# Performance work log

Measured on AMD Instinct MI355X. Metric: run time of the kernel, lower is better.

Reference implementation:

```python
import jax, jax.numpy as jnp
import numpy as np

# ---- static config (matches init_kwargs) ----
DIM = 192
HEADS = 6
DEPTH = 2
WS = (2, 7, 7)          # window / group size (Gd, Gh, Gw)
SHIFT = (1, 3, 3)       # cyclic shift for the shifted block (ws // 2)
MLP_RATIO = 4
EPS = 1e-5


def _rel_pos_index(ws):
    # same math as Attention.forward's relative_position_index construction
    coords = np.stack(np.meshgrid(np.arange(ws[0]), np.arange(ws[1]), np.arange(ws[2]), indexing='ij'))
    cf = coords.reshape(3, -1)                       # (3, N)
    rel = cf[:, :, None] - cf[:, None, :]            # (3, N, N)
    rel = rel.transpose(1, 2, 0).copy()              # (N, N, 3)
    rel[:, :, 0] += ws[0] - 1
    rel[:, :, 1] += ws[1] - 1
    rel[:, :, 2] += ws[2] - 1
    rel[:, :, 0] *= (2 * ws[1] - 1) * (2 * ws[2] - 1)
    rel[:, :, 1] *= 2 * ws[2] - 1
    return rel.sum(-1).astype(np.int32)              # (N, N)


def _np_window_partition(x, ws):
    b, d, h, w, c = x.shape
    x = x.reshape(b, d // ws[0], ws[0], h // ws[1], ws[1], w // ws[2], ws[2], c)
    return x.transpose(0, 1, 3, 5, 2, 4, 6, 7).reshape(-1, ws[0] * ws[1] * ws[2], c)


def _compute_mask(dims, ws, ss):
    # faithful to compute_mask in the source (mask value 2.0 on cross-region pairs)
    d, h, w = dims
    img_mask = np.zeros((1, d, h, w, 1), dtype=np.float32)
    cnt = 0
    for ds in (slice(-ws[0]), slice(-ws[0], -ss[0]), slice(-ss[0], None)):
        for hs in (slice(-ws[1]), slice(-ws[1], -ss[1]), slice(-ss[1], None)):
            for wsl in (slice(-ws[2]), slice(-ws[2], -ss[2]), slice(-ss[2], None)):
                img_mask[:, ds, hs, wsl, :] = cnt
                cnt += 1
    mw = _np_window_partition(img_mask, ws).squeeze(-1)   # (nW, N)
    am = mw[:, None, :] - mw[:, :, None]                  # (nW, N, N)
    return np.where(am != 0, np.float32(2.0), np.float32(0.0))


RPI = _rel_pos_index(WS)  # (N, N) int32, constant


def _ln(x, g, b):
    mu = jnp.mean(x, axis=-1, keepdims=True)
    var = jnp.mean(jnp.square(x - mu), axis=-1, keepdims=True)
    return (x - mu) * jax.lax.rsqrt(var + EPS) * g + b


def _win_part(x, ws):
    b, d, h, w, c = x.shape
    x = x.reshape(b, d // ws[0], ws[0], h // ws[1], ws[1], w // ws[2], ws[2], c)
    return x.transpose(0, 1, 3, 5, 2, 4, 6, 7).reshape(-1, ws[0] * ws[1] * ws[2], c)


def _win_rev(xw, ws, b, d, h, w):
    c = xw.shape[-1]
    x = xw.reshape(b, d // ws[0], h // ws[1], w // ws[2], ws[0], ws[1], ws[2], c)
    return x.transpose(0, 1, 4, 2, 5, 3, 6, 7).reshape(b, d, h, w, c)


def _attention(xw, qkv_w, qkv_b, proj_w, proj_b, table, mask, nW):
    B_, N, C = xw.shape
    hd = C // HEADS
    scale = hd ** -0.5
    qkv = (xw @ qkv_w.T + qkv_b).reshape(B_, N, 3, HEADS, hd).transpose(2, 0, 3, 1, 4)
    q, k, v = qkv[0] * scale, qkv[1], qkv[2]           # (B_, H, N, hd)
    attn = jnp.einsum('bhnd,bhmd->bhnm', q, k)          # (B_, H, N, N)
    bias = table[RPI.reshape(-1)].reshape(N, N, HEADS).transpose(2, 0, 1)
    attn = attn + bias[None]
    if mask is not None:
        nG = mask.shape[0]
        attn = attn.reshape(B_ // nG, nG, HEADS, N, N) + mask[None, :, None]
        attn = attn.reshape(B_, HEADS, N, N)
    attn = jax.nn.softmax(attn, axis=-1)
    out = jnp.einsum('bhnm,bhmd->bhnd', attn, v).transpose(0, 2, 1, 3).reshape(B_, N, C)
    return out @ proj_w.T + proj_b


def reference(x, ln1_g, ln1_b, qkv_w, qkv_b, proj_w, proj_b, bias_table,
              ln2_g, ln2_b, fc1_w, fc1_b, fc2_w, fc2_b):
    B, D, H, W, C = x.shape
    nW = (D // WS[0]) * (H // WS[1]) * (W // WS[2])
    shift_mask = jnp.asarray(_compute_mask((D, H, W), WS, SHIFT))
    for i in range(DEPTH):
        shifted = (i % 2 == 1)
        shortcut = x
        h = _ln(x, ln1_g[i], ln1_b[i])
        if shifted:
            h = jnp.roll(h, shift=(-SHIFT[0], -SHIFT[1], -SHIFT[2]), axis=(1, 2, 3))
        xw = _win_part(h, WS)                           # (B*nW, N, C)
        xw = _attention(xw, qkv_w[i], qkv_b[i], proj_w[i], proj_b[i],
                        bias_table[i], shift_mask if shifted else None, nW)
        h = _win_rev(xw, WS, B, D, H, W)
        if shifted:
            h = jnp.roll(h, shift=SHIFT, axis=(1, 2, 3))
        x = shortcut + h
        # MLP: Linear -> GELU -> Linear (torch GELU default = exact)
        m = _ln(x, ln2_g[i], ln2_b[i])
        m = jax.nn.gelu(m @ fc1_w[i].T + fc1_b[i], approximate=False)
        x = x + (m @ fc2_w[i].T + fc2_b[i])
    return x


def setup_inputs() -> dict:
    key = jax.random.key(0)
    ks = jax.random.split(key, 8)
    B, D, H, W, C = 2, 16, 56, 56, DIM
    hid = MLP_RATIO * C
    tbl = (2 * WS[0] - 1) * (2 * WS[1] - 1) * (2 * WS[2] - 1)
    s = 0.02
    return {
        'x': jax.random.normal(ks[0], (B, D, H, W, C), jnp.float32),
        'ln1_g': jnp.ones((DEPTH, C), jnp.float32),
        'ln1_b': jnp.zeros((DEPTH, C), jnp.float32),
        'qkv_w': jax.random.normal(ks[1], (DEPTH, 3 * C, C), jnp.float32) * s,
        'qkv_b': jnp.zeros((DEPTH, 3 * C), jnp.float32),
        'proj_w': jax.random.normal(ks[2], (DEPTH, C, C), jnp.float32) * s,
        'proj_b': jnp.zeros((DEPTH, C), jnp.float32),
        'bias_table': jax.random.normal(ks[3], (DEPTH, tbl, HEADS), jnp.float32) * s,
        'ln2_g': jnp.ones((DEPTH, C), jnp.float32),
        'ln2_b': jnp.zeros((DEPTH, C), jnp.float32),
        'fc1_w': jax.random.normal(ks[4], (DEPTH, hid, C), jnp.float32) * s,
        'fc1_b': jnp.zeros((DEPTH, hid), jnp.float32),
        'fc2_w': jax.random.normal(ks[5], (DEPTH, C, hid), jnp.float32) * s,
        'fc2_b': jnp.zeros((DEPTH, C), jnp.float32),
    }
```

## Files before the change

### kernel.cpp

```cpp
#include <hip/hip_runtime.h>
#include <math.h>

#define T_TOKENS 100352

typedef short s16x8 __attribute__((ext_vector_type(8)));
typedef float f32x4 __attribute__((ext_vector_type(4)));

__device__ __forceinline__ unsigned short f2b(float f) {
    union { float f; unsigned u; } x; x.f = f;
    unsigned r = x.u + 0x7fffu + ((x.u >> 16) & 1u);
    return (unsigned short)(r >> 16);
}
__device__ __forceinline__ float b2f(unsigned short h) {
    union { unsigned u; float f; } x; x.u = (unsigned)h << 16;
    return x.f;
}

#define GLOAD_LDS16(gsrc, ldst) __builtin_amdgcn_global_load_lds( \
    (const __attribute__((address_space(1))) void*)(gsrc), \
    (__attribute__((address_space(3))) void*)(ldst), 16, 0, 0)

__device__ __forceinline__ int win_row_to_token(int r, int shifted) {
    int widx = r / 98;
    int n = r - widx * 98;
    int b = widx >> 9;
    int remw = widx & 511;
    int dW = remw >> 6, hW = (remw >> 3) & 7, wW = remw & 7;
    int zd = n / 49;
    int nr = n - zd * 49;
    int zh = nr / 7, zw = nr - zh * 7;
    int d = dW * 2 + zd, h = hW * 7 + zh, w = wW * 7 + zw;
    if (shifted) {
        d = (d + 1) & 15;
        h += 3; if (h >= 56) h -= 56;
        w += 3; if (w >= 56) w -= 56;
    }
    return ((b * 16 + d) * 56 + h) * 56 + w;
}

__global__ __launch_bounds__(256) void f2b_kernel(
    const float* __restrict__ in, unsigned short* __restrict__ out, int n)
{
    int i = blockIdx.x * 256 + threadIdx.x;
    if (i < n) out[i] = f2b(in[i]);
}

__global__ __launch_bounds__(256) void bias_kernel(
    const float* __restrict__ table, unsigned short* __restrict__ bmc)
{
    int idx = blockIdx.x * 256 + threadIdx.x;
    if (idx >= 921984) return;
    int l = idx / 460992;
    int r = idx - l * 460992;
    int cls = r / 57624;
    int r2 = r - cls * 57624;
    int h = r2 / 9604;
    int e = r2 - h * 9604;
    int n = e / 98, m = e - n * 98;
    int zd = n / 49, nr = n - zd * 49, zh = nr / 7, zw = nr - zh * 7;
    int yd = m / 49, mr = m - yd * 49, yh = mr / 7, yw = mr - yh * 7;
    int rpi = (zd - yd + 1) * 169 + (zh - yh + 6) * 13 + (zw - yw + 6);
    float v = table[l * 3042 + rpi * 6 + h];
    int rn = (((cls >> 2) & 1) ? 1 + zd : 0) * 9
           + (((cls >> 1) & 1) ? (zh < 4 ? 1 : 2) : 0) * 3
           + ((cls & 1) ? (zw < 4 ? 1 : 2) : 0);
    int rm2 = (((cls >> 2) & 1) ? 1 + yd : 0) * 9
            + (((cls >> 1) & 1) ? (yh < 4 ? 1 : 2) : 0) * 3
            + ((cls & 1) ? (yw < 4 ? 1 : 2) : 0);
    if (rn != rm2) v += 2.0f;
    bmc[idx] = f2b(v * 1.4426950408889634f);
}

__global__ __launch_bounds__(256) void ln_kernel(
    const float* __restrict__ x, const float* __restrict__ g,
    const float* __restrict__ b, unsigned short* __restrict__ out, int mode, int row_off)
{
    int r = blockIdx.x * 4 + (threadIdx.x >> 6);
    int lane = threadIdx.x & 63;
    int t = (mode == 0) ? (row_off + r) : win_row_to_token(row_off + r, mode == 2);
    const float* xp = x + (size_t)t * 192;
    float v0 = xp[lane], v1 = xp[lane + 64], v2 = xp[lane + 128];
    float s = v0 + v1 + v2;
    float sq = v0 * v0 + v1 * v1 + v2 * v2;
    #pragma unroll
    for (int off = 32; off; off >>= 1) {
        s += __shfl_xor(s, off);
        sq += __shfl_xor(sq, off);
    }
    float mu = s * (1.0f / 192.0f);
    float var = sq * (1.0f / 192.0f) - mu * mu;
    float rs = rsqrtf(var + 1e-5f);
    unsigned short* op = out + (size_t)r * 192;
    op[lane]       = f2b((v0 - mu) * rs * g[lane]       + b[lane]);
    op[lane + 64]  = f2b((v1 - mu) * rs * g[lane + 64]  + b[lane + 64]);
    op[lane + 128] = f2b((v2 - mu) * rs * g[lane + 128] + b[lane + 128]);
}

__global__ __launch_bounds__(256) void gemm_kernel(
    const unsigned short* __restrict__ A, const unsigned short* __restrict__ Wb,
    const float* __restrict__ bias, void* outp, const float* resx,
    int N, int K, int ep, int shifted, int row_off)
{
    __shared__ __align__(16) short LDS_[128 * 64 + 96 * 64];
    short* As = LDS_;
    short* Bs = LDS_ + 128 * 64;
    const int ntiles = N / 96;
    const int NB = gridDim.x;
    int L = blockIdx.x;
    if ((NB & 7) == 0) {
        L = (blockIdx.x & 7) * (NB >> 3) + (blockIdx.x >> 3);
    }
    const int bm = L / ntiles;
    const int bn = L - bm * ntiles;
    const int r0 = bm << 7, n0 = bn * 96;
    const int tid = threadIdx.x;
    const int wid = tid >> 6, lane = tid & 63;
    const int hi = lane >> 4, l15 = lane & 15;
    const int wrow = (wid >> 1) << 6;
    const int wcol = (wid & 1) * 48;
    const int srow = lane >> 3;
    const int sslot = lane & 7;

    f32x4 acc[4][3];
    #pragma unroll
    for (int mi = 0; mi < 4; ++mi)
        #pragma unroll
        for (int ni = 0; ni < 3; ++ni)
            acc[mi][ni] = (f32x4){0.f, 0.f, 0.f, 0.f};

    for (int k0 = 0; k0 < K; k0 += 64) {
        #pragma unroll
        for (int g = 0; g < 4; ++g) {
            int row = wid * 32 + g * 8 + srow;
            const unsigned short* src =
                A + (size_t)(r0 + row) * K + k0 + ((sslot ^ (row & 7)) << 3);
            GLOAD_LDS16(src, &As[(wid * 32 + g * 8) * 64]);
        }
        #pragma unroll
        for (int g = 0; g < 3; ++g) {
            int row = wid * 24 + g * 8 + srow;
            const unsigned short* src =
                Wb + (size_t)(n0 + row) * K + k0 + ((sslot ^ (row & 7)) << 3);
            GLOAD_LDS16(src, &Bs[(wid * 24 + g * 8) * 64]);
        }
        __syncthreads();
        #pragma unroll
        for (int ks = 0; ks < 2; ++ks) {
            const int q = ks * 4 + hi;
            s16x8 bfr[3];
            #pragma unroll
            for (int ni = 0; ni < 3; ++ni) {
                int col = wcol + ni * 16 + l15;
                bfr[ni] = *(const s16x8*)&Bs[col * 64 + ((q ^ (col & 7)) << 3)];
            }
            #pragma unroll
            for (int mi = 0; mi < 4; ++mi) {
                int row = wrow + mi * 16 + l15;
                s16x8 afr = *(const s16x8*)&As[row * 64 + ((q ^ (row & 7)) << 3)];
                #pragma unroll
                for (int ni = 0; ni < 3; ++ni)
                    acc[mi][ni] = __builtin_amdgcn_mfma_f32_16x16x32_bf16(
                        afr, bfr[ni], acc[mi][ni], 0, 0, 0);
            }
        }
        __syncthreads();
    }

    if (ep <= 1) {
        #pragma unroll
        for (int mi = 0; mi < 4; ++mi)
            #pragma unroll
            for (int ni = 0; ni < 3; ++ni) {
                float bv = bias[n0 + wcol + ni * 16 + l15];
                #pragma unroll
                for (int rg = 0; rg < 4; ++rg) {
                    float v = acc[mi][ni][rg] + bv;
                    LDS_[(wrow + mi * 16 + hi * 4 + rg) * 104 + wcol + ni * 16 + l15] =
                        (short)f2b(v);
                }
            }
        __syncthreads();
        #pragma unroll
        for (int it = 0; it < 6; ++it) {
            int idx = tid + it * 256;
            int row = idx / 12, ch = idx - (idx / 12) * 12;
            s16x8 v = *(const s16x8*)&LDS_[row * 104 + ch * 8];
            *(s16x8*)&((unsigned short*)outp)[(size_t)(r0 + row) * N + n0 + ch * 8] = v;
        }
    } else {
        float* F = (float*)LDS_;
        #pragma unroll
        for (int h = 0; h < 2; ++h) {
            if ((wid >> 1) == h) {
                #pragma unroll
                for (int mi = 0; mi < 4; ++mi)
                    #pragma unroll
                    for (int ni = 0; ni < 3; ++ni) {
                        float bv = bias[n0 + wcol + ni * 16 + l15];
                        #pragma unroll
                        for (int rg = 0; rg < 4; ++rg)
                            F[(mi * 16 + hi * 4 + rg) * 100 + wcol + ni * 16 + l15] =
                                acc[mi][ni][rg] + bv;
                    }
            }
            __syncthreads();
            #pragma unroll
            for (int it = 0; it < 6; ++it) {
                int idx = tid + it * 256;
                int row = idx / 24, ch = idx - (idx / 24) * 24;
                float4 v = *(const float4*)&F[row * 100 + ch * 4];
                int rowl = r0 + h * 64 + row;
                int tt = (ep == 2) ? win_row_to_token(row_off + rowl, shifted) : rowl;
                size_t o = (size_t)tt * 192 + n0 + ch * 4;
                const float4 rx = *(const float4*)&resx[o];
                v.x += rx.x; v.y += rx.y; v.z += rx.z; v.w += rx.w;
                *(float4*)&((float*)outp)[o] = v;
            }
            __syncthreads();
        }
    }
}

__global__ __launch_bounds__(256, 4) void mlp_kernel(
    const unsigned short* __restrict__ Ab,
    const unsigned short* __restrict__ W1b,
    const float* __restrict__ b1,
    const unsigned short* __restrict__ W2b,
    const float* __restrict__ b2,
    float* out)
{
    __shared__ __align__(16) unsigned short W1c[32 * 192];
    __shared__ __align__(16) unsigned short W2c[192 * 32];
    __shared__ __align__(16) unsigned short Hb[64 * 32];

    const int tid = threadIdx.x;
    const int w = tid >> 6, lane = tid & 63;
    const int hi = lane >> 4, l15 = lane & 15;
    const int r0 = blockIdx.x << 6;
    const int arow = r0 + w * 16 + l15;

    s16x8 afr[6];
    #pragma unroll
    for (int ks = 0; ks < 6; ++ks)
        afr[ks] = *(const s16x8*)&Ab[(size_t)arow * 192 + ks * 32 + hi * 8];

    f32x4 oacc[12];
    #pragma unroll
    for (int ni = 0; ni < 12; ++ni) oacc[ni] = (f32x4){0.f, 0.f, 0.f, 0.f};

    for (int hc = 0; hc < 24; ++hc) {
        #pragma unroll
        for (int it = 0; it < 3; ++it) {
            int sbase = (w * 3 + it) * 64;
            int s = sbase + lane;
            int row = s / 24, c = s - row * 24;
            int cs = (c & 24) | ((c & 7) ^ (row & 7));
            GLOAD_LDS16(&W1b[(size_t)(hc * 32 + row) * 192 + cs * 8], &W1c[sbase * 8]);
        }
        #pragma unroll
        for (int it = 0; it < 3; ++it) {
            int sbase = (w * 3 + it) * 64;
            int s = sbase + lane;
            int row = s >> 2, sp = s & 3;
            int cs = sp ^ (row & 3);
            GLOAD_LDS16(&W2b[(size_t)row * 768 + hc * 32 + cs * 8], &W2c[sbase * 8]);
        }
        __syncthreads();

        f32x4 hacc[2];
        hacc[0] = (f32x4){0.f, 0.f, 0.f, 0.f};
        hacc[1] = (f32x4){0.f, 0.f, 0.f, 0.f};
        #pragma unroll
        for (int ks = 0; ks < 6; ++ks) {
            int slot = ks * 4 + hi;
            #pragma unroll
            for (int nc = 0; nc < 2; ++nc) {
                int col = nc * 16 + l15;
                int cs = (slot & 24) | ((slot & 7) ^ (col & 7));
                s16x8 bfr = *(const s16x8*)&W1c[col * 192 + cs * 8];
                hacc[nc] = __builtin_amdgcn_mfma_f32_16x16x32_bf16(
                    afr[ks], bfr, hacc[nc], 0, 0, 0);
            }
        }
        #pragma unroll
        for (int nc = 0; nc < 2; ++nc) {
            int col = nc * 16 + l15;
            float bv = b1[hc * 32 + col];
            int slot = col >> 3;
            #pragma unroll
            for (int rg = 0; rg < 4; ++rg) {
                float v = hacc[nc][rg] + bv;
                float y = 0.7978845608028654f * fmaf(0.044715f * v, v * v, v);
                y = fminf(fmaxf(y, -15.f), 15.f);
                float z = exp2f(2.8853900817779268f * y);
                v = v * z / (z + 1.0f);
                int row = w * 16 + hi * 4 + rg;
                Hb[row * 32 + ((slot ^ (row & 3)) << 3) + (col & 7)] = f2b(v);
            }
        }
        __syncthreads();

        {
            int cs = (hi ^ (arow & 3)) << 3;
            s16x8 pfr = *(const s16x8*)&Hb[(w * 16 + l15) * 32 + cs];
            #pragma unroll
            for (int ni = 0; ni < 12; ++ni) {
                int w2row = ni * 16 + l15;
                int cs2 = (hi ^ (w2row & 3)) << 3;
                s16x8 bfr2 = *(const s16x8*)&W2c[w2row * 32 + cs2];
                oacc[ni] = __builtin_amdgcn_mfma_f32_16x16x32_bf16(
                    pfr, bfr2, oacc[ni], 0, 0, 0);
            }
        }
        __syncthreads();
    }

    float* F = (float*)W1c;
    __syncthreads();
    {
        #pragma unroll
        for (int p = 0; p < 4; ++p) {
            if (w == p) {
                #pragma unroll
                for (int ni = 0; ni < 12; ++ni) {
                    int col = ni * 16 + l15;
                    float bv = b2[col];
                    #pragma unroll
                    for (int rg = 0; rg < 4; ++rg)
                        ((float*)W1c)[(hi * 4 + rg) * 192 + col] = oacc[ni][rg] + bv;
                }
            }
            __syncthreads();
            #pragma unroll
            for (int it = 0; it < 3; ++it) {
                int idx = tid + it * 256;
                int row = idx / 48, ch = idx - (idx / 48) * 48;
                float4 v = *(const float4*)&((float*)W1c)[row * 192 + ch * 4];
                size_t o = (size_t)(r0 + p * 16 + row) * 192 + ch * 4;
                const float4 rx = *(const float4*)&out[o];
                v.x += rx.x; v.y += rx.y; v.z += rx.z; v.w += rx.w;
                *(float4*)&out[o] = v;
            }
            __syncthreads();
        }
    }
}

__global__ __launch_bounds__(256, 4) void attn_kernel(
    const unsigned short* __restrict__ qkv, const unsigned short* __restrict__ bmc,
    unsigned short* __restrict__ out, int shifted, int widx_off)
{
    __shared__ __align__(16) short PU[112 * 136];

    const int wloc = blockIdx.x;
    const int head = blockIdx.y;
    const int tid = threadIdx.x;
    const int wid = tid >> 6, lane = tid & 63;
    const int hi = lane >> 4, l15 = lane & 15;
    const int r0 = wloc * 98;
    const float scale2 = 0.17677669529663687f * 1.4426950408889634f;

    const int remw = (widx_off + wloc) & 511;
    const int dW = remw >> 6, hW = (remw >> 3) & 7, wW = remw & 7;
    const int cls = shifted ? (((dW == 7) << 2) | ((hW == 7) << 1) | (wW == 7)) : 0;
    const unsigned short* bmch = bmc + ((size_t)cls * 6 + head) * 9604;

    for (int idx = tid; idx < 1568; idx += 256) {
        int n = idx >> 4, dp = idx & 15;
        unsigned vv = *(const unsigned*)&qkv[(size_t)(r0 + n) * 576 + 384 + head * 32 + dp * 2];
        ((unsigned short*)PU)[(2 * dp) * 136 + n]     = (unsigned short)(vv & 0xffff);
        ((unsigned short*)PU)[(2 * dp + 1) * 136 + n] = (unsigned short)(vv >> 16);
    }
    for (int idx = tid; idx < 960; idx += 256) {
        int dd = idx / 30, kvp = 98 + (idx - (idx / 30) * 30);
        ((unsigned short*)PU)[dd * 136 + kvp] = 0;
    }
    __syncthreads();

    s16x8 vfr[4][2];
    #pragma unroll
    for (int ks = 0; ks < 4; ++ks) {
        vfr[ks][0] = *(const s16x8*)&PU[(2 * l15) * 136 + ks * 32 + hi * 8];
        vfr[ks][1] = *(const s16x8*)&PU[(2 * l15 + 1) * 136 + ks * 32 + hi * 8];
    }
    s16x8 kfr[7];
    #pragma unroll
    for (int nt = 0; nt < 7; ++nt) {
        int kr = nt * 16 + l15; if (kr > 97) kr = 97;
        kfr[nt] = *(const s16x8*)&qkv[(size_t)(r0 + kr) * 576 + 192 + head * 32 + hi * 8];
    }
    __syncthreads();

    unsigned short* P = (unsigned short*)PU;
    #pragma unroll
    for (int t = 0; t < 2; ++t) {
        int mt = wid + 4 * t;
        if (mt < 7) {
            int q = mt * 16 + l15;
            int qr = q > 97 ? 97 : q;
            s16x8 qa = *(const s16x8*)&qkv[(size_t)(r0 + qr) * 576 + head * 32 + hi * 8];
            f32x4 sacc[7];
            #pragma unroll
            for (int nt = 0; nt < 7; ++nt)
                sacc[nt] = __builtin_amdgcn_mfma_f32_16x16x32_bf16(
                    kfr[nt], qa, (f32x4){0.f, 0.f, 0.f, 0.f}, 0, 0, 0);
            const int kvb = hi * 4;
            #pragma unroll
            for (int nt = 0; nt < 7; ++nt) {
                unsigned bb0 = *(const unsigned*)&bmch[qr * 98 + nt * 16 + kvb];
                unsigned bb1 = *(const unsigned*)&bmch[qr * 98 + nt * 16 + kvb + 2];
                #pragma unroll
                for (int rg = 0; rg < 4; ++rg) {
                    int kv = nt * 16 + kvb + rg;
                    unsigned bu = (rg < 2) ? bb0 : bb1;
                    float bias = b2f((unsigned short)((rg & 1) ? (bu >> 16) : (bu & 0xffffu)));
                    float val = -1e30f;
                    if (q < 98 && kv < 98)
                        val = fmaf(sacc[nt][rg], scale2, bias);
                    sacc[nt][rg] = val;
                }
            }
            float mx = sacc[0][0];
            #pragma unroll
            for (int nt = 0; nt < 7; ++nt)
                #pragma unroll
                for (int rg = 0; rg < 4; ++rg) mx = fmaxf(mx, sacc[nt][rg]);
            mx = fmaxf(mx, __shfl_xor(mx, 16));
            mx = fmaxf(mx, __shfl_xor(mx, 32));
            float sum = 0.f;
            #pragma unroll
            for (int nt = 0; nt < 7; ++nt)
                #pragma unroll
                for (int rg = 0; rg < 4; ++rg) {
                    float e = exp2f(sacc[nt][rg] - mx);
                    sacc[nt][rg] = e;
                    sum += e;
                }
            sum += __shfl_xor(sum, 16);
            sum += __shfl_xor(sum, 32);
            float inv = 1.0f / sum;
            #pragma unroll
            for (int nt = 0; nt < 7; ++nt) {
                uint2 wv;
                wv.x = (unsigned)f2b(sacc[nt][0] * inv) | ((unsigned)f2b(sacc[nt][1] * inv) << 16);
                wv.y = (unsigned)f2b(sacc[nt][2] * inv) | ((unsigned)f2b(sacc[nt][3] * inv) << 16);
                *(uint2*)&P[q * 136 + nt * 16 + kvb] = wv;
            }
            if (hi == 0) {
                const s16x8 z8 = (s16x8){0, 0, 0, 0, 0, 0, 0, 0};
                *(s16x8*)&P[q * 136 + 112] = z8;
                *(s16x8*)&P[q * 136 + 120] = z8;
            }
        }
    }
    __syncthreads();

    #pragma unroll
    for (int t = 0; t < 2; ++t) {
        int mt = wid + 4 * t;
        if (mt < 7) {
            f32x4 o0 = {0.f, 0.f, 0.f, 0.f}, o1 = {0.f, 0.f, 0.f, 0.f};
            const short* prow = &PU[(mt * 16 + l15) * 136 + hi * 8];
            #pragma unroll
            for (int ks = 0; ks < 4; ++ks) {
                s16x8 pa = *(const s16x8*)&prow[ks * 32];
                o0 = __builtin_amdgcn_mfma_f32_16x16x32_bf16(pa, vfr[ks][0], o0, 0, 0, 0);
                o1 = __builtin_amdgcn_mfma_f32_16x16x32_bf16(pa, vfr[ks][1], o1, 0, 0, 0);
            }
            #pragma unroll
            for (int rg = 0; rg < 4; ++rg) {
                int q = mt * 16 + hi * 4 + rg;
                if (q < 98) {
                    unsigned pv = (unsigned)f2b(o0[rg]) | ((unsigned)f2b(o1[rg]) << 16);
                    *(unsigned*)&out[(size_t)(r0 + q) * 192 + head * 32 + 2 * l15] = pv;
                }
            }
        }
    }
}

extern "C" void kernel_launch(void* const* d_in, const int* in_sizes, int n_in,
                              void* d_out, int out_size, void* d_ws, size_t ws_size,
                              hipStream_t stream) {
    (void)in_sizes; (void)n_in; (void)out_size;
    const float* x      = (const float*)d_in[0];
    const float* ln1_g  = (const float*)d_in[1];
    const float* ln1_b  = (const float*)d_in[2];
    const float* qkv_w  = (const float*)d_in[3];
    const float* qkv_b  = (const float*)d_in[4];
    const float* proj_w = (const float*)d_in[5];
    const float* proj_b = (const float*)d_in[6];
    const float* table  = (const float*)d_in[7];
    const float* ln2_g  = (const float*)d_in[8];
    const float* ln2_b  = (const float*)d_in[9];
    const float* fc1_w  = (const float*)d_in[10];
    const float* fc1_b  = (const float*)d_in[11];
    const float* fc2_w  = (const float*)d_in[12];
    const float* fc2_b  = (const float*)d_in[13];
    float* out = (float*)d_out;

    const int NQ = 576 * 192, NP = 192 * 192, N1 = 768 * 192, N2 = 192 * 768;
    const size_t WTOT = 2ull * (NQ + NP + N1 + N2);
    unsigned short* wq = (unsigned short*)d_ws;
    unsigned short* wp = wq + 2 * NQ;
    unsigned short* w1 = wp + 2 * NP;
    unsigned short* w2 = w1 + 2 * N1;
    unsigned short* bmc = wq + WTOT;
    unsigned short* bufbase = bmc + 921984;
    const size_t fixed_bytes = (WTOT + 921984) * 2;

    const size_t per_win_bytes = 98ull * (192 + 576) * sizeof(unsigned short);
    int wpc = 64;
    const int cands[5] = {1024, 512, 256, 128, 64};
    for (int ci = 0; ci < 5; ++ci) {
        if (fixed_bytes + (size_t)cands[ci] * per_win_bytes <= ws_size) { wpc = cands[ci]; break; }
    }
    const int NC = 1024 / wpc;
    const int CR = 98 * wpc;
    unsigned short* bufA = bufbase;
    unsigned short* bufQ = bufA + (size_t)CR * 192;

    f2b_kernel<<<(2 * NQ + 255) / 256, 256, 0, stream>>>(qkv_w,  wq, 2 * NQ);
    f2b_kernel<<<(2 * NP + 255) / 256, 256, 0, stream>>>(proj_w, wp, 2 * NP);
    f2b_kernel<<<(2 * N1 + 255) / 256, 256, 0, stream>>>(fc1_w,  w1, 2 * N1);
    f2b_kernel<<<(2 * N2 + 255) / 256, 256, 0, stream>>>(fc2_w,  w2, 2 * N2);
    bias_kernel<<<(921984 + 255) / 256, 256, 0, stream>>>(table, bmc);

    for (int i = 0; i < 2; ++i) {
        const int shifted = (i == 1);
        const float* xsrc = (i == 0) ? x : out;
        for (int c = 0; c < NC; ++c) {
            const int row_off = c * CR;
            const int widx_off = c * wpc;
            ln_kernel<<<CR / 4, 256, 0, stream>>>(
                xsrc, ln1_g + i * 192, ln1_b + i * 192, bufA, shifted ? 2 : 1, row_off);
            gemm_kernel<<<(CR / 128) * 6, 256, 0, stream>>>(
                bufA, wq + (size_t)i * NQ, qkv_b + i * 576,
                bufQ, nullptr, 576, 192, 0, 0, 0);
            attn_kernel<<<dim3(wpc, 6), 256, 0, stream>>>(
                bufQ, bmc + (size_t)i * 460992, bufA, shifted, widx_off);
            gemm_kernel<<<(CR / 128) * 2, 256, 0, stream>>>(
                bufA, wp + (size_t)i * NP, proj_b + i * 192,
                out, xsrc, 192, 192, 2, shifted, row_off);
        }
        for (int c = 0; c < NC; ++c) {
            const int row_off = c * CR;
            ln_kernel<<<CR / 4, 256, 0, stream>>>(
                out, ln2_g + i * 192, ln2_b + i * 192, bufA, 0, row_off);
            mlp_kernel<<<CR / 64, 256, 0, stream>>>(
                bufA, w1 + (size_t)i * N1, fc1_b + (size_t)i * 768,
                w2 + (size_t)i * N2, fc2_b + (size_t)i * 192,
                out + (size_t)row_off * 192);
        }
    }
}
```

Baseline: 742.7 us.

## Restructure MLP kernel LDS layouts to k-slot-major and transpose fc1 MFMA

Changes the shared-memory layout of the W1 and W2 weight chunks from XOR-swizzled row-major to a k-slot-major layout, so each lane reads a contiguous 16-byte fragment without swizzle arithmetic. The fc1 MFMA operands are swapped so each lane holds four consecutive hidden columns for one token. That lets the GELU results be packed into a single 8-byte store into a padded (stride-40) hidden buffer instead of four scalar 2-byte stores. It also removes one redundant barrier before the epilogue. The risk is LDS bank conflicts in the new unswizzled layouts, and the W1 chunk is padded buffer-size-wise but used unswizzled.

```diff
diff --git a/kernel.cpp b/kernel.cpp
--- a/kernel.cpp
+++ b/kernel.cpp
@@ -229,9 +229,9 @@
     const float* __restrict__ b2,
     float* out)
 {
-    __shared__ __align__(16) unsigned short W1c[32 * 192];
-    __shared__ __align__(16) unsigned short W2c[192 * 32];
-    __shared__ __align__(16) unsigned short Hb[64 * 32];
+    __shared__ __align__(16) unsigned short W1c[24 * 32 * 8];
+    __shared__ __align__(16) unsigned short W2c[4 * 192 * 8];
+    __shared__ __align__(16) unsigned short Hb[64 * 40];
 
     const int tid = threadIdx.x;
     const int w = tid >> 6, lane = tid & 63;
@@ -252,18 +252,17 @@
         #pragma unroll
         for (int it = 0; it < 3; ++it) {
             int sbase = (w * 3 + it) * 64;
-            int s = sbase + lane;
-            int row = s / 24, c = s - row * 24;
-            int cs = (c & 24) | ((c & 7) ^ (row & 7));
-            GLOAD_LDS16(&W1b[(size_t)(hc * 32 + row) * 192 + cs * 8], &W1c[sbase * 8]);
+            int u = sbase + lane;
+            GLOAD_LDS16(&W1b[(size_t)(hc * 32 + (u & 31)) * 192 + (u >> 5) * 8],
+                        &W1c[sbase * 8]);
         }
         #pragma unroll
         for (int it = 0; it < 3; ++it) {
             int sbase = (w * 3 + it) * 64;
-            int s = sbase + lane;
-            int row = s >> 2, sp = s & 3;
-            int cs = sp ^ (row & 3);
-            GLOAD_LDS16(&W2b[(size_t)row * 768 + hc * 32 + cs * 8], &W2c[sbase * 8]);
+            int u = sbase + lane;
+            int ks2 = u / 192, row = u - ks2 * 192;
+            GLOAD_LDS16(&W2b[(size_t)row * 768 + hc * 32 + ks2 * 8],
+                        &W2c[sbase * 8]);
         }
         __syncthreads();
 
@@ -275,39 +274,41 @@
             int slot = ks * 4 + hi;
             #pragma unroll
             for (int nc = 0; nc < 2; ++nc) {
-                int col = nc * 16 + l15;
-                int cs = (slot & 24) | ((slot & 7) ^ (col & 7));
-                s16x8 bfr = *(const s16x8*)&W1c[col * 192 + cs * 8];
+                s16x8 wfr = *(const s16x8*)&W1c[(slot * 32 + nc * 16 + l15) * 8];
                 hacc[nc] = __builtin_amdgcn_mfma_f32_16x16x32_bf16(
-                    afr[ks], bfr, hacc[nc], 0, 0, 0);
+                    wfr, afr[ks], hacc[nc], 0, 0, 0);
             }
         }
         #pragma unroll
         for (int nc = 0; nc < 2; ++nc) {
-            int col = nc * 16 + l15;
-            float bv = b1[hc * 32 + col];
-            int slot = col >> 3;
-            #pragma unroll
-            for (int rg = 0; rg < 4; ++rg) {
-                float v = hacc[nc][rg] + bv;
-                float y = 0.7978845608028654f * fmaf(0.044715f * v, v * v, v);
-                y = fminf(fmaxf(y, -15.f), 15.f);
-                float z = exp2f(2.8853900817779268f * y);
-                v = v * z / (z + 1.0f);
-                int row = w * 16 + hi * 4 + rg;
-                Hb[row * 32 + ((slot ^ (row & 3)) << 3) + (col & 7)] = f2b(v);
-            }
+            const float4 bv4 = *(const float4*)&b1[hc * 32 + nc * 16 + hi * 4];
+            float bvs[4] = {bv4.x, bv4.y, bv4.z, bv4.w};
+            unsigned pk[2];
+            #pragma unroll
+            for (int pr = 0; pr < 2; ++pr) {
+                unsigned short lo, hi2;
+                #pragma unroll
+                for (int k2 = 0; k2 < 2; ++k2) {
+                    int rg = pr * 2 + k2;
+                    float v = hacc[nc][rg] + bvs[rg];
+                    float y = 0.7978845608028654f * fmaf(0.044715f * v, v * v, v);
+                    y = fminf(fmaxf(y, -15.f), 15.f);
+                    float z = exp2f(2.8853900817779268f * y);
+                    v = v * z / (z + 1.0f);
+                    if (k2 == 0) lo = f2b(v); else hi2 = f2b(v);
+                }
+                pk[pr] = (unsigned)lo | ((unsigned)hi2 << 16);
+            }
+            int token = w * 16 + l15;
+            *(uint2*)&Hb[token * 40 + nc * 16 + hi * 4] = make_uint2(pk[0], pk[1]);
         }
         __syncthreads();
 
         {
-            int cs = (hi ^ (arow & 3)) << 3;
-            s16x8 pfr = *(const s16x8*)&Hb[(w * 16 + l15) * 32 + cs];
+            s16x8 pfr = *(const s16x8*)&Hb[(w * 16 + l15) * 40 + hi * 8];
             #pragma unroll
             for (int ni = 0; ni < 12; ++ni) {
-                int w2row = ni * 16 + l15;
-                int cs2 = (hi ^ (w2row & 3)) << 3;
-                s16x8 bfr2 = *(const s16x8*)&W2c[w2row * 32 + cs2];
+                s16x8 bfr2 = *(const s16x8*)&W2c[(hi * 192 + ni * 16 + l15) * 8];
                 oacc[ni] = __builtin_amdgcn_mfma_f32_16x16x32_bf16(
                     pfr, bfr2, oacc[ni], 0, 0, 0);
             }
@@ -315,34 +316,30 @@
         __syncthreads();
     }
 
-    float* F = (float*)W1c;
-    __syncthreads();
-    {
-        #pragma unroll
-        for (int p = 0; p < 4; ++p) {
-            if (w == p) {
-                #pragma unroll
-                for (int ni = 0; ni < 12; ++ni) {
-                    int col = ni * 16 + l15;
-                    float bv = b2[col];
-                    #pragma unroll
-                    for (int rg = 0; rg < 4; ++rg)
-                        ((float*)W1c)[(hi * 4 + rg) * 192 + col] = oacc[ni][rg] + bv;
-                }
-            }
-            __syncthreads();
-            #pragma unroll
-            for (int it = 0; it < 3; ++it) {
-                int idx = tid + it * 256;
-                int row = idx / 48, ch = idx - (idx / 48) * 48;
-                float4 v = *(const float4*)&((float*)W1c)[row * 192 + ch * 4];
-                size_t o = (size_t)(r0 + p * 16 + row) * 192 + ch * 4;
-                const float4 rx = *(const float4*)&out[o];
-                v.x += rx.x; v.y += rx.y; v.z += rx.z; v.w += rx.w;
-                *(float4*)&out[o] = v;
-            }
-            __syncthreads();
-        }
+    #pragma unroll
+    for (int p = 0; p < 4; ++p) {
+        if (w == p) {
+            #pragma unroll
+            for (int ni = 0; ni < 12; ++ni) {
+                int col = ni * 16 + l15;
+                float bv = b2[col];
+                #pragma unroll
+                for (int rg = 0; rg < 4; ++rg)
+                    ((float*)W1c)[(hi * 4 + rg) * 192 + col] = oacc[ni][rg] + bv;
+            }
+        }
+        __syncthreads();
+        #pragma unroll
+        for (int it = 0; it < 3; ++it) {
+            int idx = tid + it * 256;
+            int row = idx / 48, ch = idx - (idx / 48) * 48;
+            float4 v = *(const float4*)&((float*)W1c)[row * 192 + ch * 4];
+            size_t o = (size_t)(r0 + p * 16 + row) * 192 + ch * 4;
+            const float4 rx = *(const float4*)&out[o];
+            v.x += rx.x; v.y += rx.y; v.z += rx.z; v.w += rx.w;
+            *(float4*)&out[o] = v;
+        }
+        __syncthreads();
     }
 }
 
```

Result: slower. 818.3 us (+10.2%).
